# Optimization experiments

Measured on AMD Instinct MI355X. Metric: run time of the kernel, lower is better.

## Reference

```python
import jax, jax.numpy as jnp
import numpy as np

N_NODES = 50000
N_EDGES = 800000
IN_DIM, HID_DIM, OUT_DIM = 64, 128, 128


def _glorot(key, shape):
    fan_in, fan_out = shape[1], shape[0]
    lim = float(np.sqrt(6.0 / (fan_in + fan_out)))
    return jax.random.uniform(key, shape, jnp.float32, -lim, lim)


def setup_inputs() -> dict:
    key = jax.random.key(0)
    ks = jax.random.split(key, 8)
    x = jax.random.normal(ks[0], (N_NODES, IN_DIM), jnp.float32)
    edge_index = jax.random.randint(ks[1], (2, N_EDGES), 0, N_NODES, jnp.int64)
    return {
        "x": x,
        "edge_index": edge_index,
        # layer 1 (SAGEConv: lin_l acts on aggregated neighbors + bias, lin_r on root)
        "W1_l": _glorot(ks[2], (HID_DIM, IN_DIM)),
        "W1_r": _glorot(ks[3], (HID_DIM, IN_DIM)),
        "b1": jnp.zeros((HID_DIM,), jnp.float32),
        # layer 2
        "W2_l": _glorot(ks[4], (OUT_DIM, HID_DIM)),
        "W2_r": _glorot(ks[5], (OUT_DIM, HID_DIM)),
        "b2": jnp.zeros((OUT_DIM,), jnp.float32),
    }


def _sage_conv(x, src, dst, W_l, W_r, b):
    # mean aggregation of neighbor features: messages flow src -> dst
    msg = x[src]                                           # [E, D]
    agg = jax.ops.segment_sum(msg, dst, num_segments=N_NODES)  # [N, D]
    deg = jax.ops.segment_sum(jnp.ones((msg.shape[0],), x.dtype), dst,
                              num_segments=N_NODES)        # [N]
    mean = agg / jnp.maximum(deg, 1.0)[:, None]            # isolated nodes -> 0
    return mean @ W_l.T + x @ W_r.T + b


def reference(x, edge_index, W1_l, W1_r, b1, W2_l, W2_r, b2):
    src, dst = edge_index[0], edge_index[1]
    h = _sage_conv(x, src, dst, W1_l, W1_r, b1)
    h = jax.nn.relu(h)
    out = _sage_conv(h, src, dst, W2_l, W2_r, b2)
    return out
```

## Files before the change

### kernel.cpp

```cpp
#include <hip/hip_runtime.h>
#include <hip/hip_bf16.h>

constexpr int N  = 50000;
constexpr int E  = 800000;
constexpr int D0 = 64;
constexpr int D1 = 128;
constexpr int CAP = 64;

constexpr int NPART = 8;
constexpr int PSZ   = (N + NPART - 1) / NPART;
constexpr int BPP   = 128;

typedef __attribute__((ext_vector_type(8))) short short8;
typedef __attribute__((ext_vector_type(4))) float f32x4;

__device__ __forceinline__ unsigned short bf16bits(float f) {
    __hip_bfloat16 hb = __float2bfloat16(f);
    return *reinterpret_cast<unsigned short*>(&hb);
}

__device__ __forceinline__ void acc8(float* a, const uint4 r) {
    union { unsigned u; float f; } c;
    c.u = r.x << 16;         a[0] += c.f;
    c.u = r.x & 0xffff0000u; a[1] += c.f;
    c.u = r.y << 16;         a[2] += c.f;
    c.u = r.y & 0xffff0000u; a[3] += c.f;
    c.u = r.z << 16;         a[4] += c.f;
    c.u = r.z & 0xffff0000u; a[5] += c.f;
    c.u = r.w << 16;         a[6] += c.f;
    c.u = r.w & 0xffff0000u; a[7] += c.f;
}

__global__ __launch_bounds__(256)
void k_bin(const int* __restrict__ src, const int* __restrict__ dst,
           int* __restrict__ cnt, int* __restrict__ bin) {
    const int p     = blockIdx.x & (NPART - 1);
    const int local = blockIdx.x >> 3;
    const int lo = p * PSZ;
    const int hi = min(N, lo + PSZ);

    for (int i = local * 256 + threadIdx.x; i < E / 4; i += BPP * 256) {
        const int e0 = i * 4;
        int4 d = *(const int4*)&dst[e0];
        int4 s = *(const int4*)&src[e0];
        if (d.x >= lo && d.x < hi) {
            int pos = atomicAdd(&cnt[d.x], 1);
            if (pos < CAP) bin[d.x * CAP + pos] = s.x;
        }
        if (d.y >= lo && d.y < hi) {
            int pos = atomicAdd(&cnt[d.y], 1);
            if (pos < CAP) bin[d.y * CAP + pos] = s.y;
        }
        if (d.z >= lo && d.z < hi) {
            int pos = atomicAdd(&cnt[d.z], 1);
            if (pos < CAP) bin[d.z * CAP + pos] = s.z;
        }
        if (d.w >= lo && d.w < hi) {
            int pos = atomicAdd(&cnt[d.w], 1);
            if (pos < CAP) bin[d.w * CAP + pos] = s.w;
        }
    }
}

__global__ void k_cvtx(const float* __restrict__ x, unsigned short* __restrict__ xb) {
    int i = blockIdx.x * blockDim.x + threadIdx.x;
    if (i >= N * D0 / 8) return;
    const float4 v0 = *(const float4*)&x[(size_t)i * 8];
    const float4 v1 = *(const float4*)&x[(size_t)i * 8 + 4];
    float f[8] = {v0.x, v0.y, v0.z, v0.w, v1.x, v1.y, v1.z, v1.w};
    unsigned short u[8];
    #pragma unroll
    for (int j = 0; j < 8; ++j) u[j] = bf16bits(f[j]);
    *(short8*)&xb[(size_t)i * 8] = *(short8*)u;
}

__global__ void k_wprep(const float* __restrict__ W1l, const float* __restrict__ W1r,
                        const float* __restrict__ W2l, const float* __restrict__ W2r,
                        unsigned short* __restrict__ W1cat,
                        unsigned short* __restrict__ W2cat) {
    int i = blockIdx.x * blockDim.x + threadIdx.x;
    if (i < 128 * 128) {
        int o = i >> 7, k = i & 127;
        float v = (k < 64) ? W1l[o * 64 + k] : W1r[o * 64 + (k - 64)];
        W1cat[i] = bf16bits(v);
    }
    if (i < 128 * 256) {
        int o = i >> 8, k = i & 255;
        float v = (k < 128) ? W2l[o * 128 + k] : W2r[o * 128 + (k - 128)];
        W2cat[i] = bf16bits(v);
    }
}

template<int DIN>
__global__ __launch_bounds__(256, 8)
void k_gather(const unsigned short* __restrict__ xin,
              const int* __restrict__ cnt,
              const int* __restrict__ bin,
              unsigned short* __restrict__ mean) {
    constexpr int GRPSZ = DIN / 8;
    constexpr int GPB   = 256 / GRPSZ;
    const int tid      = threadIdx.x;
    const int sub      = tid & (GRPSZ - 1);
    const int gloc     = tid / GRPSZ;
    const int lane     = tid & 63;
    const int lanebase = (lane / GRPSZ) * GRPSZ;
    const int g0   = blockIdx.x * GPB + gloc;
    const int gstr = gridDim.x * GPB;

    for (int n = g0; n < N; n += gstr) {
        const int deg  = cnt[n];
        const int degc = min(deg, CAP);
        const int base = n * CAP;

        float a[8] = {0.f, 0.f, 0.f, 0.f, 0.f, 0.f, 0.f, 0.f};

        for (int b = 0; b < degc; b += GRPSZ) {
            int nb = (b + sub < degc) ? bin[base + b + sub] : 0;
            const int c = min(GRPSZ, degc - b);
            int j = 0;
            for (; j + 4 <= c; j += 4) {
                int s0 = __shfl(nb, lanebase + j + 0);
                int s1 = __shfl(nb, lanebase + j + 1);
                int s2 = __shfl(nb, lanebase + j + 2);
                int s3 = __shfl(nb, lanebase + j + 3);
                uint4 r0 = *(const uint4*)&xin[(size_t)s0 * DIN + sub * 8];
                uint4 r1 = *(const uint4*)&xin[(size_t)s1 * DIN + sub * 8];
                uint4 r2 = *(const uint4*)&xin[(size_t)s2 * DIN + sub * 8];
                uint4 r3 = *(const uint4*)&xin[(size_t)s3 * DIN + sub * 8];
                acc8(a, r0); acc8(a, r1); acc8(a, r2); acc8(a, r3);
            }
            for (; j < c; ++j) {
                int s = __shfl(nb, lanebase + j);
                uint4 r = *(const uint4*)&xin[(size_t)s * DIN + sub * 8];
                acc8(a, r);
            }
        }

        const float invd = 1.0f / fmaxf((float)deg, 1.0f);
        unsigned short u[8];
        #pragma unroll
        for (int q = 0; q < 8; ++q) u[q] = bf16bits(a[q] * invd);
        *(short8*)&mean[(size_t)n * DIN + sub * 8] = *(short8*)u;
    }
}

template<int DIN, bool RELU, bool OUT_BF16>
__global__ __launch_bounds__(256)
void k_mdense(const unsigned short* __restrict__ mean,
              const unsigned short* __restrict__ xin,
              const unsigned short* __restrict__ Wcat,
              const float* __restrict__ bias,
              void* __restrict__ out,
              int n_nodes) {
    constexpr int K  = 2 * DIN;
    constexpr int KP = K + 8;
    __shared__ unsigned short A[64 * KP];

    const int tid   = threadIdx.x;
    const int nbase = blockIdx.x * 64;

    constexpr int CPR   = K / 8;
    constexpr int TOTAL = 64 * CPR;
    for (int c = tid; c < TOTAL; c += 256) {
        int row  = c / CPR;
        int col8 = (c - row * CPR) * 8;
        int n    = nbase + row;
        short8 v = (short8)0;
        if (n < n_nodes) {
            const unsigned short* srcp = (col8 < DIN)
                ? &mean[(size_t)n * DIN + col8]
                : &xin[(size_t)n * DIN + (col8 - DIN)];
            v = *(const short8*)srcp;
        }
        *(short8*)&A[row * KP + col8] = v;
    }
    __syncthreads();

    const int lane = tid & 63;
    const int wv   = tid >> 6;
    const int l15  = lane & 15;
    const int kseg = lane >> 4;

    f32x4 acc[8];
    #pragma unroll
    for (int ot = 0; ot < 8; ++ot) acc[ot] = (f32x4){0.f, 0.f, 0.f, 0.f};

    #pragma unroll
    for (int kk = 0; kk < K / 32; ++kk) {
        short8 a = *(const short8*)&A[(wv * 16 + l15) * KP + kk * 32 + kseg * 8];
        #pragma unroll
        for (int ot = 0; ot < 8; ++ot) {
            short8 b = *(const short8*)&Wcat[(size_t)(ot * 16 + l15) * K + kk * 32 + kseg * 8];
            acc[ot] = __builtin_amdgcn_mfma_f32_16x16x32_bf16(a, b, acc[ot], 0, 0, 0);
        }
    }

    #pragma unroll
    for (int ot = 0; ot < 8; ++ot) {
        const int o  = ot * 16 + l15;
        const float bv = bias[o];
        #pragma unroll
        for (int i = 0; i < 4; ++i) {
            int n = nbase + wv * 16 + kseg * 4 + i;
            if (n < n_nodes) {
                float v = acc[ot][i] + bv;
                if constexpr (RELU) v = fmaxf(v, 0.0f);
                if constexpr (OUT_BF16) {
                    ((unsigned short*)out)[(size_t)n * 128 + o] = bf16bits(v);
                } else {
                    ((float*)out)[(size_t)n * 128 + o] = v;
                }
            }
        }
    }
}

extern "C" void kernel_launch(void* const* d_in, const int* in_sizes, int n_in,
                              void* d_out, int out_size, void* d_ws, size_t ws_size,
                              hipStream_t stream) {
    const float* x   = (const float*)d_in[0];
    const int*   ei  = (const int*)d_in[1];
    const float* W1l = (const float*)d_in[2];
    const float* W1r = (const float*)d_in[3];
    const float* b1  = (const float*)d_in[4];
    const float* W2l = (const float*)d_in[5];
    const float* W2r = (const float*)d_in[6];
    const float* b2  = (const float*)d_in[7];
    float*       out = (float*)d_out;

    const int* src = ei;
    const int* dst = ei + E;

    char* p = (char*)d_ws;
    auto alloc = [&](size_t bytes) -> char* {
        char* r = p; p += (bytes + 15) & ~(size_t)15; return r;
    };
    int*            cnt   = (int*)alloc(N * sizeof(int));
    int*            bin   = (int*)alloc((size_t)N * CAP * sizeof(int));
    unsigned short* xb    = (unsigned short*)alloc((size_t)N * D0 * 2);
    unsigned short* h     = (unsigned short*)alloc((size_t)N * D1 * 2);
    unsigned short* mean  = (unsigned short*)alloc((size_t)N * D1 * 2);
    unsigned short* W1cat = (unsigned short*)alloc(128 * 128 * 2);
    unsigned short* W2cat = (unsigned short*)alloc(128 * 256 * 2);

    const int nblk_d = (N + 63) / 64;

    k_cvtx<<<(N * D0 / 8 + 255) / 256, 256, 0, stream>>>(x, xb);
    k_wprep<<<(128 * 256 + 255) / 256, 256, 0, stream>>>(W1l, W1r, W2l, W2r, W1cat, W2cat);

    hipMemsetAsync(cnt, 0, (size_t)N * sizeof(int), stream);
    k_bin<<<NPART * BPP, 256, 0, stream>>>(src, dst, cnt, bin);

    k_gather<D0><<<2048, 256, 0, stream>>>(xb, cnt, bin, mean);
    k_mdense<D0, true, true>
        <<<nblk_d, 256, 0, stream>>>(mean, xb, W1cat, b1, h, N);

    k_gather<D1><<<2048, 256, 0, stream>>>(h, cnt, bin, mean);
    k_mdense<D1, false, false>
        <<<nblk_d, 256, 0, stream>>>(mean, h, W2cat, b2, out, N);
}
```

Measured before the change: 173.1 us.

## Two-pass partitioned edge binning with packed 16-bit indices and fused prep kernel

```diff
diff --git a/kernel.cpp b/kernel.cpp
--- a/kernel.cpp
+++ b/kernel.cpp
@@ -10,6 +10,10 @@
 constexpr int NPART = 8;
 constexpr int PSZ   = (N + NPART - 1) / NPART;
 constexpr int BPP   = 128;
+constexpr int PCAP  = 131072;
+constexpr int CAPB  = 768;
+constexpr int ABLK  = 256;
+constexpr int EPB   = E / ABLK;
 
 typedef __attribute__((ext_vector_type(8))) short short8;
 typedef __attribute__((ext_vector_type(4))) float f32x4;
@@ -32,53 +36,14 @@
 }
 
 __global__ __launch_bounds__(256)
-void k_bin(const int* __restrict__ src, const int* __restrict__ dst,
-           int* __restrict__ cnt, int* __restrict__ bin) {
-    const int p     = blockIdx.x & (NPART - 1);
-    const int local = blockIdx.x >> 3;
-    const int lo = p * PSZ;
-    const int hi = min(N, lo + PSZ);
-
-    for (int i = local * 256 + threadIdx.x; i < E / 4; i += BPP * 256) {
-        const int e0 = i * 4;
-        int4 d = *(const int4*)&dst[e0];
-        int4 s = *(const int4*)&src[e0];
-        if (d.x >= lo && d.x < hi) {
-            int pos = atomicAdd(&cnt[d.x], 1);
-            if (pos < CAP) bin[d.x * CAP + pos] = s.x;
-        }
-        if (d.y >= lo && d.y < hi) {
-            int pos = atomicAdd(&cnt[d.y], 1);
-            if (pos < CAP) bin[d.y * CAP + pos] = s.y;
-        }
-        if (d.z >= lo && d.z < hi) {
-            int pos = atomicAdd(&cnt[d.z], 1);
-            if (pos < CAP) bin[d.z * CAP + pos] = s.z;
-        }
-        if (d.w >= lo && d.w < hi) {
-            int pos = atomicAdd(&cnt[d.w], 1);
-            if (pos < CAP) bin[d.w * CAP + pos] = s.w;
-        }
-    }
-}
-
-__global__ void k_cvtx(const float* __restrict__ x, unsigned short* __restrict__ xb) {
+void k_prep(const float* __restrict__ x, unsigned short* __restrict__ xb,
+            const float* __restrict__ W1l, const float* __restrict__ W1r,
+            const float* __restrict__ W2l, const float* __restrict__ W2r,
+            unsigned short* __restrict__ W1cat, unsigned short* __restrict__ W2cat,
+            int* __restrict__ cnt, int* __restrict__ pcnt) {
     int i = blockIdx.x * blockDim.x + threadIdx.x;
-    if (i >= N * D0 / 8) return;
-    const float4 v0 = *(const float4*)&x[(size_t)i * 8];
-    const float4 v1 = *(const float4*)&x[(size_t)i * 8 + 4];
-    float f[8] = {v0.x, v0.y, v0.z, v0.w, v1.x, v1.y, v1.z, v1.w};
-    unsigned short u[8];
-    #pragma unroll
-    for (int j = 0; j < 8; ++j) u[j] = bf16bits(f[j]);
-    *(short8*)&xb[(size_t)i * 8] = *(short8*)u;
-}
-
-__global__ void k_wprep(const float* __restrict__ W1l, const float* __restrict__ W1r,
-                        const float* __restrict__ W2l, const float* __restrict__ W2r,
-                        unsigned short* __restrict__ W1cat,
-                        unsigned short* __restrict__ W2cat) {
-    int i = blockIdx.x * blockDim.x + threadIdx.x;
+    if (i < NPART) pcnt[i] = 0;
+    if (i < N / 4) ((int4*)cnt)[i] = make_int4(0, 0, 0, 0);
     if (i < 128 * 128) {
         int o = i >> 7, k = i & 127;
         float v = (k < 64) ? W1l[o * 64 + k] : W1r[o * 64 + (k - 64)];
@@ -89,13 +54,80 @@
         float v = (k < 128) ? W2l[o * 128 + k] : W2r[o * 128 + (k - 128)];
         W2cat[i] = bf16bits(v);
     }
+    if (i < N * D0 / 8) {
+        const float4 v0 = *(const float4*)&x[(size_t)i * 8];
+        const float4 v1 = *(const float4*)&x[(size_t)i * 8 + 4];
+        float f[8] = {v0.x, v0.y, v0.z, v0.w, v1.x, v1.y, v1.z, v1.w};
+        unsigned short u[8];
+        #pragma unroll
+        for (int j = 0; j < 8; ++j) u[j] = bf16bits(f[j]);
+        *(short8*)&xb[(size_t)i * 8] = *(short8*)u;
+    }
+}
+
+__global__ __launch_bounds__(256)
+void k_binA(const int* __restrict__ src, const int* __restrict__ dst,
+            int* __restrict__ pcnt, unsigned* __restrict__ parts) {
+    __shared__ unsigned buck[NPART][CAPB];
+    __shared__ int bcnt[NPART];
+    __shared__ int bbase[NPART];
+    const int tid = threadIdx.x;
+    if (tid < NPART) bcnt[tid] = 0;
+    __syncthreads();
+
+    const int e_lo = blockIdx.x * EPB;
+    const int e_hi = e_lo + EPB;
+    for (int e = e_lo + tid; e < e_hi; e += 256) {
+        int d = dst[e];
+        int s = src[e];
+        int p = d / PSZ;
+        unsigned v = ((unsigned)d << 16) | (unsigned)s;
+        int pos = atomicAdd(&bcnt[p], 1);
+        if (pos < CAPB) {
+            buck[p][pos] = v;
+        } else {
+            int g = atomicAdd(&pcnt[p], 1);
+            if (g < PCAP) parts[(size_t)p * PCAP + g] = v;
+        }
+    }
+    __syncthreads();
+
+    if (tid < NPART) {
+        int c = min(bcnt[tid], CAPB);
+        bbase[tid] = atomicAdd(&pcnt[tid], c);
+        bcnt[tid] = c;
+    }
+    __syncthreads();
+
+    for (int p = 0; p < NPART; ++p) {
+        const int c = bcnt[p], base = bbase[p];
+        for (int i = tid; i < c; i += 256) {
+            int g = base + i;
+            if (g < PCAP) parts[(size_t)p * PCAP + g] = buck[p][i];
+        }
+    }
+}
+
+__global__ __launch_bounds__(256)
+void k_binB(const int* __restrict__ pcnt, const unsigned* __restrict__ parts,
+            int* __restrict__ cnt, unsigned short* __restrict__ bin) {
+    const int p     = blockIdx.x & (NPART - 1);
+    const int local = blockIdx.x >> 3;
+    const int K = min(pcnt[p], PCAP);
+    for (int i = local * 256 + threadIdx.x; i < K; i += BPP * 256) {
+        unsigned v = parts[(size_t)p * PCAP + i];
+        int d = (int)(v >> 16);
+        int s = (int)(v & 0xffffu);
+        int pos = atomicAdd(&cnt[d], 1);
+        if (pos < CAP) bin[(size_t)d * CAP + pos] = (unsigned short)s;
+    }
 }
 
 template<int DIN>
 __global__ __launch_bounds__(256, 8)
 void k_gather(const unsigned short* __restrict__ xin,
               const int* __restrict__ cnt,
-              const int* __restrict__ bin,
+              const unsigned short* __restrict__ bin,
               unsigned short* __restrict__ mean) {
     constexpr int GRPSZ = DIN / 8;
     constexpr int GPB   = 256 / GRPSZ;
@@ -110,12 +142,12 @@
     for (int n = g0; n < N; n += gstr) {
         const int deg  = cnt[n];
         const int degc = min(deg, CAP);
-        const int base = n * CAP;
+        const size_t base = (size_t)n * CAP;
 
         float a[8] = {0.f, 0.f, 0.f, 0.f, 0.f, 0.f, 0.f, 0.f};
 
         for (int b = 0; b < degc; b += GRPSZ) {
-            int nb = (b + sub < degc) ? bin[base + b + sub] : 0;
+            int nb = (b + sub < degc) ? (int)bin[base + b + sub] : 0;
             const int c = min(GRPSZ, degc - b);
             int j = 0;
             for (; j + 4 <= c; j += 4) {
@@ -236,7 +268,9 @@
         char* r = p; p += (bytes + 15) & ~(size_t)15; return r;
     };
     int*            cnt   = (int*)alloc(N * sizeof(int));
-    int*            bin   = (int*)alloc((size_t)N * CAP * sizeof(int));
+    int*            pcnt  = (int*)alloc(NPART * sizeof(int));
+    unsigned*       parts = (unsigned*)alloc((size_t)NPART * PCAP * sizeof(unsigned));
+    unsigned short* bin   = (unsigned short*)alloc((size_t)N * CAP * 2);
     unsigned short* xb    = (unsigned short*)alloc((size_t)N * D0 * 2);
     unsigned short* h     = (unsigned short*)alloc((size_t)N * D1 * 2);
     unsigned short* mean  = (unsigned short*)alloc((size_t)N * D1 * 2);
@@ -245,11 +279,11 @@
 
     const int nblk_d = (N + 63) / 64;
 
-    k_cvtx<<<(N * D0 / 8 + 255) / 256, 256, 0, stream>>>(x, xb);
-    k_wprep<<<(128 * 256 + 255) / 256, 256, 0, stream>>>(W1l, W1r, W2l, W2r, W1cat, W2cat);
-
-    hipMemsetAsync(cnt, 0, (size_t)N * sizeof(int), stream);
-    k_bin<<<NPART * BPP, 256, 0, stream>>>(src, dst, cnt, bin);
+    k_prep<<<(N * D0 / 8 + 255) / 256, 256, 0, stream>>>(
+        x, xb, W1l, W1r, W2l, W2r, W1cat, W2cat, cnt, pcnt);
+
+    k_binA<<<ABLK, 256, 0, stream>>>(src, dst, pcnt, parts);
+    k_binB<<<NPART * BPP, 256, 0, stream>>>(pcnt, parts, cnt, bin);
 
     k_gather<D0><<<2048, 256, 0, stream>>>(xb, cnt, bin, mean);
     k_mdense<D0, true, true>
```

Measured after the change: 175.7 us. About the same (+1.5%).
